# Kernel optimization log

Hardware: AMD Instinct MI355X
Metric: run time of the kernel (lower is better)

## Reference

```python
import jax, jax.numpy as jnp
import numpy as np

TAU = 2.0        # spikingjelly LIFNode default tau
ALPHA = 4.0      # sigmoid surrogate alpha (spikingjelly default)
NUM_HEADS = 8
CHUNK = 2

@jax.custom_vjp
def heaviside(x):
    return (x >= 0).astype(x.dtype)

def _h_fwd(x):
    return heaviside(x), x

def _h_bwd(x, g):
    s = jax.nn.sigmoid(ALPHA * x)
    return (g * ALPHA * s * (1.0 - s),)

heaviside.defvjp(_h_fwd, _h_bwd)

def lif(x, v_th):
    # multi-step LIF: v <- v + (x - v)/tau ; spike = H(v - v_th) ; hard reset to 0
    def step(v, xt):
        v = v + (xt - v) / TAU
        s = heaviside(v - v_th)
        return v * (1.0 - s), s
    _, spikes = jax.lax.scan(step, jnp.zeros_like(x[0]), x)
    return spikes

def bn(x, p, eps=1e-5):
    # eval-mode BatchNorm1d over channel dim C of [T,B,C,V]; p = [gamma,beta,mean,var] each [C]
    g, b, m, v = p[0], p[1], p[2], p[3]
    scale = g * jax.lax.rsqrt(v + eps)
    return (x - m[:, None]) * scale[:, None] + b[:, None]

def setup_inputs() -> dict:
    key = jax.random.key(0)
    T, B, C, V = 8, 16, 256, 1024
    ks = jax.random.split(key, 10)
    def mk_bn(k):
        k1, k2, k3, k4 = jax.random.split(k, 4)
        return jnp.stack([
            jax.random.uniform(k1, (C,)) + 0.5,          # gamma
            0.1 * jax.random.normal(k2, (C,)),           # beta
            0.1 * jax.random.normal(k3, (C,)),           # running mean
            jax.random.uniform(k4, (C,)) * 0.5 + 0.5,    # running var (>0)
        ])
    w_scale = C ** -0.5
    return {
        "x": jax.random.normal(ks[0], (T, B, C, V), jnp.float32),
        "q_w": w_scale * jax.random.normal(ks[1], (C, C), jnp.float32),
        "k_w": w_scale * jax.random.normal(ks[2], (C, C), jnp.float32),
        "v_w": w_scale * jax.random.normal(ks[3], (C, C), jnp.float32),
        "proj_w": w_scale * jax.random.normal(ks[4], (C, C), jnp.float32),
        "proj_b": 0.01 * jax.random.normal(ks[5], (C,), jnp.float32),
        "bn_q": mk_bn(ks[6]),
        "bn_k": mk_bn(ks[7]),
        "bn_v": mk_bn(ks[8]),
        "bn_proj": mk_bn(ks[9]),
    }

def reference(x, q_w, k_w, v_w, proj_w, proj_b, bn_q, bn_k, bn_v, bn_proj):
    T, B, C, V = x.shape
    H = NUM_HEADS
    D = C // H
    N = V
    NC = T // CHUNK
    identity = x

    xs = lif(x, 1.0)  # shortcut_lif

    def branch(w, bnp):
        y = jnp.einsum('oc,tbcv->tbov', w, xs)   # 1x1 conv
        y = lif(bn(y, bnp), 1.0)
        # [T,B,C,V] -> [T,B,H,N,D]
        return y.transpose(0, 1, 3, 2).reshape(T, B, N, H, D).transpose(0, 1, 3, 2, 4)

    q = branch(q_w, bn_q)
    k = branch(k_w, bn_k)
    v = branch(v_w, bn_v)

    def chunk(t):
        # [T,B,H,N,D] -> [NC,B,H,CHUNK*N,D]
        return (t.reshape(NC, CHUNK, B, H, N, D)
                 .transpose(0, 2, 3, 1, 4, 5)
                 .reshape(NC, B, H, CHUNK * N, D))

    qc, kc, vc = chunk(q), chunk(k), chunk(v)
    attn = jnp.einsum('nbhld,nbhle->nbhde', kc, vc) * (1.0 / N)  # [NC,B,H,D,D]
    out = jnp.einsum('nbhld,nbhde->nbhle', qc, attn)             # [NC,B,H,CHUNK*N,D]
    out = (out.reshape(NC, B, H, CHUNK, N, D)
              .transpose(0, 3, 1, 2, 4, 5)
              .reshape(T, B, H, N, D))

    y = out.transpose(0, 1, 2, 4, 3).reshape(T, B, C, N)  # [T,B,H,D,N] -> [T,B,C,N]
    y = lif(y, 0.5)  # attn_lif
    y = jnp.einsum('oc,tbcv->tbov', proj_w, y) + proj_b[None, None, :, None]
    y = bn(y, bn_proj)
    return y + identity, v
```

## Files before the change

kernel.cpp:

```cpp
#include <hip/hip_runtime.h>
#include <hip/hip_bf16.h>
#include <math.h>

typedef __bf16 bf16_t;
typedef __bf16 bf16x8 __attribute__((ext_vector_type(8)));
typedef __bf16 bf16x4 __attribute__((ext_vector_type(4)));
typedef float  f32x4  __attribute__((ext_vector_type(4)));

#define T_ 8
#define B_ 16
#define C_ 256
#define V_ 1024
#define H_ 8
#define D_ 32

#define MFMA __builtin_amdgcn_mfma_f32_16x16x32_bf16

__global__ __launch_bounds__(256) void k0_split4(const float* __restrict__ W0,
                                                 const float* __restrict__ W1,
                                                 const float* __restrict__ W2,
                                                 const float* __restrict__ W3,
                                                 bf16_t* __restrict__ S)
{
    const int mat = blockIdx.x >> 6;
    const float* W = (mat == 0) ? W0 : (mat == 1) ? W1 : (mat == 2) ? W2 : W3;
    bf16_t* S0 = S + (size_t)mat * 3 * 65536;
    bf16_t* S1 = S0 + 65536;
    bf16_t* S2 = S0 + 131072;
    int i = ((blockIdx.x & 63) * 256 + threadIdx.x) * 4;
    float4 w = *(const float4*)(W + i);
    float wv[4] = {w.x, w.y, w.z, w.w};
    bf16x4 s0, s1, s2;
#pragma unroll
    for (int j = 0; j < 4; j++) {
        bf16_t a = (bf16_t)wv[j];
        float r1 = wv[j] - (float)a;
        bf16_t b = (bf16_t)r1;
        float r2 = r1 - (float)b;
        bf16_t c = (bf16_t)r2;
        s0[j] = a; s1[j] = b; s2[j] = c;
    }
    *(bf16x4*)(S0 + i) = s0;
    *(bf16x4*)(S1 + i) = s1;
    *(bf16x4*)(S2 + i) = s2;
}

__global__ __launch_bounds__(256) void k1_lif_tr(const float* __restrict__ x,
                                                 bf16_t* __restrict__ xsT)
{
    __shared__ bf16_t tile[64 * 72];
    const int v0 = blockIdx.x * 64, c0 = blockIdx.y * 64, b = blockIdx.z;
    const int tid = threadIdx.x;
    const int cc = tid >> 2, v16 = (tid & 3) * 16;
    const int vr = tid >> 2, c16 = (tid & 3) * 16;
    float mem[16];
#pragma unroll
    for (int j = 0; j < 16; j++) mem[j] = 0.0f;

    for (int t = 0; t < T_; t++) {
        const float* xp = x + (((size_t)(t * B_ + b) * C_ + (c0 + cc)) * V_ + v0 + v16);
        float xv[16];
#pragma unroll
        for (int q = 0; q < 4; q++) {
            float4 f = *(const float4*)(xp + q * 4);
            xv[q * 4 + 0] = f.x; xv[q * 4 + 1] = f.y;
            xv[q * 4 + 2] = f.z; xv[q * 4 + 3] = f.w;
        }
#pragma unroll
        for (int j = 0; j < 16; j++) {
            float m = mem[j];
            float d = xv[j] - m;
            m = m + d * 0.5f;
            float s = (m >= 1.0f) ? 1.0f : 0.0f;
            tile[(v16 + j) * 72 + cc] = (bf16_t)s;
            mem[j] = (s != 0.0f) ? 0.0f : m;
        }
        __syncthreads();
        bf16_t* op = xsT + (((size_t)(t * B_ + b) * V_ + (v0 + vr)) * C_ + c0 + c16);
        *(bf16x8*)op       = *(const bf16x8*)&tile[vr * 72 + c16];
        *(bf16x8*)(op + 8) = *(const bf16x8*)&tile[vr * 72 + c16 + 8];
        __syncthreads();
    }
}

template <int ORIENT>
__global__ __launch_bounds__(256, 2) void k_branch(const bf16_t* __restrict__ Wsp,
                                                   const float* __restrict__ bnp,
                                                   const bf16_t* __restrict__ xsT,
                                                   bf16_t* __restrict__ outp, float vth)
{
    __shared__ bf16_t Wl[3][64 * 40];
    __shared__ bf16_t Xl[8][64 * 40];
    __shared__ float bsc[64], bmn[64], bbt[64];
    const int v0 = blockIdx.x * 64, o0 = blockIdx.y * 64, b = blockIdx.z;
    const int tid = threadIdx.x;
    const int w = tid >> 6, l = tid & 63, lq = l >> 4, lr = l & 15;
    const int msub = (w >> 1) * 32, nsub = (w & 1) * 32;

    if (tid < 64) {
        int o = o0 + tid;
        float g = bnp[o], be = bnp[C_ + o];
        float mn = bnp[2 * C_ + o], vr2 = bnp[3 * C_ + o];
        bsc[tid] = g * (1.0f / sqrtf(vr2 + 1e-5f));
        bmn[tid] = mn; bbt[tid] = be;
    }

    f32x4 acc[8][4];
#pragma unroll
    for (int t = 0; t < 8; t++)
#pragma unroll
        for (int i = 0; i < 4; i++) acc[t][i] = (f32x4){0.f, 0.f, 0.f, 0.f};

    for (int kq = 0; kq < 8; kq++) {
        __syncthreads();
#pragma unroll
        for (int i = 0; i < 3; i++) {
            int ch = tid + i * 256;
            int lvl = ch >> 8, rem = ch & 255;
            int row = rem >> 2, col8 = (rem & 3) * 8;
            *(bf16x8*)&Wl[lvl][row * 40 + col8] =
                *(const bf16x8*)&Wsp[lvl * 65536 + (o0 + row) * 256 + kq * 32 + col8];
        }
#pragma unroll
        for (int i = 0; i < 8; i++) {
            int ch = tid + i * 256;
            int tt = ch >> 8, rem = ch & 255;
            int row = rem >> 2, col8 = (rem & 3) * 8;
            *(bf16x8*)&Xl[tt][row * 40 + col8] =
                *(const bf16x8*)&xsT[((size_t)(tt * B_ + b) * V_ + v0 + row) * C_ + kq * 32 + col8];
        }
        __syncthreads();

        bf16x8 aw0[3], aw1[3];
#pragma unroll
        for (int lvl = 0; lvl < 3; lvl++) {
            aw0[lvl] = *(const bf16x8*)&Wl[lvl][(msub + lr) * 40 + lq * 8];
            aw1[lvl] = *(const bf16x8*)&Wl[lvl][(msub + 16 + lr) * 40 + lq * 8];
        }
#pragma unroll
        for (int t = 0; t < 8; t++) {
            bf16x8 b0 = *(const bf16x8*)&Xl[t][(nsub + lr) * 40 + lq * 8];
            bf16x8 b1 = *(const bf16x8*)&Xl[t][(nsub + 16 + lr) * 40 + lq * 8];
#pragma unroll
            for (int lvl = 0; lvl < 3; lvl++) {
                if (ORIENT == 0) {
                    acc[t][0] = MFMA(aw0[lvl], b0, acc[t][0], 0, 0, 0);
                    acc[t][1] = MFMA(aw0[lvl], b1, acc[t][1], 0, 0, 0);
                    acc[t][2] = MFMA(aw1[lvl], b0, acc[t][2], 0, 0, 0);
                    acc[t][3] = MFMA(aw1[lvl], b1, acc[t][3], 0, 0, 0);
                } else {
                    acc[t][0] = MFMA(b0, aw0[lvl], acc[t][0], 0, 0, 0);
                    acc[t][1] = MFMA(b1, aw0[lvl], acc[t][1], 0, 0, 0);
                    acc[t][2] = MFMA(b0, aw1[lvl], acc[t][2], 0, 0, 0);
                    acc[t][3] = MFMA(b1, aw1[lvl], acc[t][3], 0, 0, 0);
                }
            }
        }
    }

    __syncthreads();
    bf16_t* tl = (bf16_t*)Xl;
    const int orow = tid >> 2, ocol = (tid & 3) * 16;
    float mem[4][4];
#pragma unroll
    for (int st = 0; st < 4; st++)
#pragma unroll
        for (int r = 0; r < 4; r++) mem[st][r] = 0.0f;
#pragma unroll
    for (int t = 0; t < 8; t++) {
#pragma unroll
        for (int st = 0; st < 4; st++) {
            int mi = st >> 1, ni = st & 1;
#pragma unroll
            for (int r = 0; r < 4; r++) {
                int m, n;
                if (ORIENT == 0) {
                    m = msub + mi * 16 + lq * 4 + r;
                    n = nsub + ni * 16 + lr;
                } else {
                    m = msub + mi * 16 + lr;
                    n = nsub + ni * 16 + lq * 4 + r;
                }
                float y = (acc[t][st][r] - bmn[m]) * bsc[m] + bbt[m];
                float mm = mem[st][r];
                mm = mm + (y - mm) * 0.5f;
                float s = (mm >= vth) ? 1.0f : 0.0f;
                mem[st][r] = (s != 0.0f) ? 0.0f : mm;
                if (ORIENT == 0) tl[m * 72 + n] = (bf16_t)s;
                else             tl[n * 72 + m] = (bf16_t)s;
            }
        }
        __syncthreads();
        size_t rowbase;
        if (ORIENT == 0)
            rowbase = ((size_t)(t * B_ + b) * C_ + (o0 + orow)) * V_ + v0 + ocol;
        else
            rowbase = ((size_t)(t * B_ + b) * V_ + (v0 + orow)) * C_ + o0 + ocol;
        *(bf16x8*)&outp[rowbase]     = *(const bf16x8*)&tl[orow * 72 + ocol];
        *(bf16x8*)&outp[rowbase + 8] = *(const bf16x8*)&tl[orow * 72 + ocol + 8];
        __syncthreads();
    }
}

__global__ __launch_bounds__(256) void k_attn(const bf16_t* __restrict__ vc,
                                              const bf16_t* __restrict__ kc,
                                              bf16_t* __restrict__ ahi,
                                              bf16_t* __restrict__ alo)
{
    __shared__ float red[3][64][20];
    const int fid = blockIdx.x;
    const int h = fid & 7, b = (fid >> 3) & 15, nc = fid >> 7;
    const int tid = threadIdx.x, w = tid >> 6, l = tid & 63, lq = l >> 4, lr = l & 15;
    f32x4 acc[4];
#pragma unroll
    for (int i = 0; i < 4; i++) acc[i] = (f32x4){0.f, 0.f, 0.f, 0.f};
    for (int ss = 0; ss < 16; ss++) {
        int s = w * 16 + ss;
        int t = nc * 2 + (s >> 5);
        int n0 = (s & 31) * 32;
        size_t rb = ((size_t)(t * B_ + b) * C_ + h * D_ + lr) * V_ + n0 + lq * 8;
        bf16x8 a0 = *(const bf16x8*)&vc[rb];
        bf16x8 a1 = *(const bf16x8*)&vc[rb + (size_t)16 * V_];
        bf16x8 b0 = *(const bf16x8*)&kc[rb];
        bf16x8 b1 = *(const bf16x8*)&kc[rb + (size_t)16 * V_];
        acc[0] = MFMA(a0, b0, acc[0], 0, 0, 0);
        acc[1] = MFMA(a0, b1, acc[1], 0, 0, 0);
        acc[2] = MFMA(a1, b0, acc[2], 0, 0, 0);
        acc[3] = MFMA(a1, b1, acc[3], 0, 0, 0);
    }
    if (w) {
#pragma unroll
        for (int st = 0; st < 4; st++)
            *(f32x4*)&red[w - 1][l][st * 4] = acc[st];
    }
    __syncthreads();
    if (w == 0) {
#pragma unroll
        for (int st = 0; st < 4; st++)
#pragma unroll
            for (int i = 0; i < 3; i++)
                acc[st] += *(const f32x4*)&red[i][l][st * 4];

        size_t ob = (size_t)fid * 1024;
#pragma unroll
        for (int st = 0; st < 4; st++) {
            int ei = st >> 1, di = st & 1;
#pragma unroll
            for (int r = 0; r < 4; r++) {
                int e = ei * 16 + lq * 4 + r;
                int d = di * 16 + lr;
                float val = acc[st][r] * (1.0f / 1024.0f);
                bf16_t hi = (bf16_t)val;
                float lo = val - (float)hi;
                ahi[ob + e * 32 + d] = hi;
                alo[ob + e * 32 + d] = (bf16_t)lo;
            }
        }
    }
}

__global__ __launch_bounds__(256) void k_attn_out(const bf16_t* __restrict__ qT,
                                                  const bf16_t* __restrict__ ahi,
                                                  const bf16_t* __restrict__ alo,
                                                  bf16_t* __restrict__ y3T)
{
    const int tid = threadIdx.x, w = tid >> 6, l = tid & 63, lq = l >> 4, lr = l & 15;
    const int n0 = blockIdx.x * 64 + (w >> 1) * 32;
    const int h = blockIdx.y * 2 + (w & 1);
    const int b = blockIdx.z;
    float mem[4][4];
#pragma unroll
    for (int st = 0; st < 4; st++)
#pragma unroll
        for (int r = 0; r < 4; r++) mem[st][r] = 0.0f;

    for (int t = 0; t < T_; t++) {
        int nc = t >> 1;
        const bf16_t* qp = qT + ((size_t)(t * B_ + b) * V_ + n0 + lr) * C_ + h * D_ + lq * 8;
        bf16x8 a0 = *(const bf16x8*)qp;
        bf16x8 a1 = *(const bf16x8*)(qp + 16 * C_);
        size_t ab = ((size_t)(nc * B_ + b) * H_ + h) * 1024;
        bf16x8 bh0 = *(const bf16x8*)&ahi[ab + lr * 32 + lq * 8];
        bf16x8 bh1 = *(const bf16x8*)&ahi[ab + (16 + lr) * 32 + lq * 8];
        bf16x8 bl0 = *(const bf16x8*)&alo[ab + lr * 32 + lq * 8];
        bf16x8 bl1 = *(const bf16x8*)&alo[ab + (16 + lr) * 32 + lq * 8];
#pragma unroll
        for (int st = 0; st < 4; st++) {
            int mi = st >> 1, ni = st & 1;
            f32x4 z = (f32x4){0.f, 0.f, 0.f, 0.f};
            z = MFMA(mi ? a1 : a0, ni ? bh1 : bh0, z, 0, 0, 0);
            z = MFMA(mi ? a1 : a0, ni ? bl1 : bl0, z, 0, 0, 0);
#pragma unroll
            for (int r = 0; r < 4; r++) {
                int n = n0 + mi * 16 + lq * 4 + r;
                int e = ni * 16 + lr;
                float mm = mem[st][r];
                mm = mm + (z[r] - mm) * 0.5f;
                float s = (mm >= 0.5f) ? 1.0f : 0.0f;
                y3T[((size_t)(t * B_ + b) * V_ + n) * C_ + h * D_ + e] = (bf16_t)s;
                mem[st][r] = (s != 0.0f) ? 0.0f : mm;
            }
        }
    }
}

__global__ __launch_bounds__(256, 2) void k_proj(const bf16_t* __restrict__ Wsp,
                                                 const float* __restrict__ pb,
                                                 const float* __restrict__ bnp,
                                                 const bf16_t* __restrict__ y3T,
                                                 const float* __restrict__ x,
                                                 float* __restrict__ out0)
{
    __shared__ bf16_t Wl[3][64 * 40];
    __shared__ bf16_t Xl[8][64 * 40];
    __shared__ float bsc[64], bmn[64], bbt[64], bbi[64];
    const int v0 = blockIdx.x * 64, o0 = blockIdx.y * 64, b = blockIdx.z;
    const int tid = threadIdx.x;
    const int w = tid >> 6, l = tid & 63, lq = l >> 4, lr = l & 15;
    const int msub = (w >> 1) * 32, nsub = (w & 1) * 32;

    if (tid < 64) {
        int o = o0 + tid;
        float g = bnp[o], be = bnp[C_ + o];
        float mn = bnp[2 * C_ + o], vr2 = bnp[3 * C_ + o];
        bsc[tid] = g * (1.0f / sqrtf(vr2 + 1e-5f));
        bmn[tid] = mn; bbt[tid] = be; bbi[tid] = pb[o];
    }

    f32x4 acc[8][4];
#pragma unroll
    for (int t = 0; t < 8; t++)
#pragma unroll
        for (int i = 0; i < 4; i++) acc[t][i] = (f32x4){0.f, 0.f, 0.f, 0.f};

    for (int kq = 0; kq < 8; kq++) {
        __syncthreads();
#pragma unroll
        for (int i = 0; i < 3; i++) {
            int ch = tid + i * 256;
            int lvl = ch >> 8, rem = ch & 255;
            int row = rem >> 2, col8 = (rem & 3) * 8;
            *(bf16x8*)&Wl[lvl][row * 40 + col8] =
                *(const bf16x8*)&Wsp[lvl * 65536 + (o0 + row) * 256 + kq * 32 + col8];
        }
#pragma unroll
        for (int i = 0; i < 8; i++) {
            int ch = tid + i * 256;
            int tt = ch >> 8, rem = ch & 255;
            int row = rem >> 2, col8 = (rem & 3) * 8;
            *(bf16x8*)&Xl[tt][row * 40 + col8] =
                *(const bf16x8*)&y3T[((size_t)(tt * B_ + b) * V_ + v0 + row) * C_ + kq * 32 + col8];
        }
        __syncthreads();

        bf16x8 aw0[3], aw1[3];
#pragma unroll
        for (int lvl = 0; lvl < 3; lvl++) {
            aw0[lvl] = *(const bf16x8*)&Wl[lvl][(msub + lr) * 40 + lq * 8];
            aw1[lvl] = *(const bf16x8*)&Wl[lvl][(msub + 16 + lr) * 40 + lq * 8];
        }
#pragma unroll
        for (int t = 0; t < 8; t++) {
            bf16x8 b0 = *(const bf16x8*)&Xl[t][(nsub + lr) * 40 + lq * 8];
            bf16x8 b1 = *(const bf16x8*)&Xl[t][(nsub + 16 + lr) * 40 + lq * 8];
#pragma unroll
            for (int lvl = 0; lvl < 3; lvl++) {
                acc[t][0] = MFMA(aw0[lvl], b0, acc[t][0], 0, 0, 0);
                acc[t][1] = MFMA(aw0[lvl], b1, acc[t][1], 0, 0, 0);
                acc[t][2] = MFMA(aw1[lvl], b0, acc[t][2], 0, 0, 0);
                acc[t][3] = MFMA(aw1[lvl], b1, acc[t][3], 0, 0, 0);
            }
        }
    }

    __syncthreads();
    float* tf = (float*)Xl;
    const int orow = tid >> 2, ocol = (tid & 3) * 16;
#pragma unroll
    for (int t = 0; t < 8; t++) {
#pragma unroll
        for (int st = 0; st < 4; st++) {
            int mi = st >> 1, ni = st & 1;
#pragma unroll
            for (int r = 0; r < 4; r++) {
                int m = msub + mi * 16 + lq * 4 + r;
                int n = nsub + ni * 16 + lr;
                float y = acc[t][st][r] + bbi[m];
                y = (y - bmn[m]) * bsc[m] + bbt[m];
                tf[m * 68 + n] = y;
            }
        }
        __syncthreads();
        size_t rowbase = ((size_t)(t * B_ + b) * C_ + (o0 + orow)) * V_ + v0 + ocol;
#pragma unroll
        for (int q = 0; q < 4; q++) {
            float4 xv = *(const float4*)&x[rowbase + q * 4];
            float4 yv = *(const float4*)&tf[orow * 68 + ocol + q * 4];
            yv.x += xv.x; yv.y += xv.y; yv.z += xv.z; yv.w += xv.w;
            *(float4*)&out0[rowbase + q * 4] = yv;
        }
        __syncthreads();
    }
}

__global__ __launch_bounds__(256) void k_vout(const bf16_t* __restrict__ vc,
                                              float* __restrict__ out1)
{
    __shared__ bf16_t tl[32 * 136];
    const int n0 = blockIdx.x * 128;
    const int f = blockIdx.y;
    const int tb = f >> 3, h = f & 7;
    const int tid = threadIdx.x;
    {
        int d = tid >> 3, nn = (tid & 7) * 16;
        const bf16_t* vp = vc + ((size_t)tb * C_ + h * D_ + d) * V_ + n0 + nn;
        *(bf16x8*)&tl[d * 136 + nn]     = *(const bf16x8*)vp;
        *(bf16x8*)&tl[d * 136 + nn + 8] = *(const bf16x8*)(vp + 8);
    }
    __syncthreads();
    {
        int n = tid >> 1, d16 = (tid & 1) * 16;
        float* op = out1 + (size_t)f * (V_ * D_) + (size_t)(n0 + n) * D_ + d16;
#pragma unroll
        for (int q = 0; q < 4; q++) {
            float4 o;
            o.x = (float)tl[(d16 + q * 4 + 0) * 136 + n];
            o.y = (float)tl[(d16 + q * 4 + 1) * 136 + n];
            o.z = (float)tl[(d16 + q * 4 + 2) * 136 + n];
            o.w = (float)tl[(d16 + q * 4 + 3) * 136 + n];
            *(float4*)(op + q * 4) = o;
        }
    }
}

extern "C" void kernel_launch(void* const* d_in, const int* in_sizes, int n_in,
                              void* d_out, int out_size, void* d_ws, size_t ws_size,
                              hipStream_t stream)
{
    const float* x    = (const float*)d_in[0];
    const float* q_w  = (const float*)d_in[1];
    const float* k_w  = (const float*)d_in[2];
    const float* v_w  = (const float*)d_in[3];
    const float* pw   = (const float*)d_in[4];
    const float* pb   = (const float*)d_in[5];
    const float* bn_q = (const float*)d_in[6];
    const float* bn_k = (const float*)d_in[7];
    const float* bn_v = (const float*)d_in[8];
    const float* bn_p = (const float*)d_in[9];

    char* ws = (char*)d_ws;
    bf16_t* xsT  = (bf16_t*)(ws);
    bf16_t* vc   = (bf16_t*)(ws + ((size_t)64 << 20));
    bf16_t* ahi  = (bf16_t*)(ws + ((size_t)128 << 20));
    bf16_t* alo  = (bf16_t*)(ws + ((size_t)129 << 20));
    bf16_t* wspq = (bf16_t*)(ws + ((size_t)130 << 20));
    bf16_t* wspk = wspq + 3 * 65536;
    bf16_t* wspv = wspk + 3 * 65536;
    bf16_t* wspp = wspv + 3 * 65536;
    bf16_t* y3T  = xsT;

    float* outf = (float*)d_out;
    bf16_t* qT = (bf16_t*)d_out;
    bf16_t* kc = (bf16_t*)((char*)d_out + ((size_t)64 << 20));

    k0_split4  <<<dim3(256),        256, 0, stream>>>(q_w, k_w, v_w, pw, wspq);
    k1_lif_tr  <<<dim3(16, 4, 16),  256, 0, stream>>>(x, xsT);
    k_branch<1><<<dim3(16, 4, 16),  256, 0, stream>>>(wspq, bn_q, xsT, qT, 1.0f);
    k_branch<0><<<dim3(16, 4, 16),  256, 0, stream>>>(wspk, bn_k, xsT, kc, 1.0f);
    k_branch<0><<<dim3(16, 4, 16),  256, 0, stream>>>(wspv, bn_v, xsT, vc, 1.0f);
    k_attn     <<<dim3(512),        256, 0, stream>>>(vc, kc, ahi, alo);
    k_attn_out <<<dim3(16, 4, 16),  256, 0, stream>>>(qT, ahi, alo, y3T);
    k_proj     <<<dim3(16, 4, 16),  256, 0, stream>>>(wspp, pb, bn_p, y3T, x, outf);
    k_vout     <<<dim3(8, 1024),    256, 0, stream>>>(vc, outf + (size_t)33554432);
}
```

Baseline: 696.5 us.

## Load MFMA operands directly from global memory instead of LDS staging

In the branch and projection GEMM kernels, the shared-memory staging of weight and spike tiles is removed. Each wave now loads its MFMA A/B fragments straight from global memory (bf16x8 per lane), and the two barriers per K-step are dropped. Shared memory shrinks to just the epilogue transpose tile, which could allow more blocks per CU. In exchange, each operand is fetched redundantly by several waves, and the loads are strided 16-byte row accesses that rely on L1/L2 hits rather than coalesced LDS fills.

After: 893.3 us. 28.2% more time.

```diff
diff --git a/kernel.cpp b/kernel.cpp
--- a/kernel.cpp
+++ b/kernel.cpp
@@ -89,8 +89,7 @@
                                                    const bf16_t* __restrict__ xsT,
                                                    bf16_t* __restrict__ outp, float vth)
 {
-    __shared__ bf16_t Wl[3][64 * 40];
-    __shared__ bf16_t Xl[8][64 * 40];
+    __shared__ bf16_t tl[64 * 72];
     __shared__ float bsc[64], bmn[64], bbt[64];
     const int v0 = blockIdx.x * 64, o0 = blockIdx.y * 64, b = blockIdx.z;
     const int tid = threadIdx.x;
@@ -111,36 +110,24 @@
 #pragma unroll
         for (int i = 0; i < 4; i++) acc[t][i] = (f32x4){0.f, 0.f, 0.f, 0.f};
 
+    const bf16_t* wr0 = Wsp + (o0 + msub + lr) * 256;
+    const bf16_t* wr1 = Wsp + (o0 + msub + 16 + lr) * 256;
+    const size_t xrow0 = ((size_t)v0 + nsub + lr) * C_;
+    const size_t xrow1 = ((size_t)v0 + nsub + 16 + lr) * C_;
+
     for (int kq = 0; kq < 8; kq++) {
-        __syncthreads();
-#pragma unroll
-        for (int i = 0; i < 3; i++) {
-            int ch = tid + i * 256;
-            int lvl = ch >> 8, rem = ch & 255;
-            int row = rem >> 2, col8 = (rem & 3) * 8;
-            *(bf16x8*)&Wl[lvl][row * 40 + col8] =
-                *(const bf16x8*)&Wsp[lvl * 65536 + (o0 + row) * 256 + kq * 32 + col8];
-        }
-#pragma unroll
-        for (int i = 0; i < 8; i++) {
-            int ch = tid + i * 256;
-            int tt = ch >> 8, rem = ch & 255;
-            int row = rem >> 2, col8 = (rem & 3) * 8;
-            *(bf16x8*)&Xl[tt][row * 40 + col8] =
-                *(const bf16x8*)&xsT[((size_t)(tt * B_ + b) * V_ + v0 + row) * C_ + kq * 32 + col8];
-        }
-        __syncthreads();
-
+        const int kc8 = kq * 32 + lq * 8;
         bf16x8 aw0[3], aw1[3];
 #pragma unroll
         for (int lvl = 0; lvl < 3; lvl++) {
-            aw0[lvl] = *(const bf16x8*)&Wl[lvl][(msub + lr) * 40 + lq * 8];
-            aw1[lvl] = *(const bf16x8*)&Wl[lvl][(msub + 16 + lr) * 40 + lq * 8];
+            aw0[lvl] = *(const bf16x8*)&wr0[lvl * 65536 + kc8];
+            aw1[lvl] = *(const bf16x8*)&wr1[lvl * 65536 + kc8];
         }
 #pragma unroll
         for (int t = 0; t < 8; t++) {
-            bf16x8 b0 = *(const bf16x8*)&Xl[t][(nsub + lr) * 40 + lq * 8];
-            bf16x8 b1 = *(const bf16x8*)&Xl[t][(nsub + 16 + lr) * 40 + lq * 8];
+            const bf16_t* xb = xsT + (size_t)(t * B_ + b) * (V_ * C_) + kc8;
+            bf16x8 b0 = *(const bf16x8*)&xb[xrow0];
+            bf16x8 b1 = *(const bf16x8*)&xb[xrow1];
 #pragma unroll
             for (int lvl = 0; lvl < 3; lvl++) {
                 if (ORIENT == 0) {
@@ -158,8 +145,6 @@
         }
     }
 
-    __syncthreads();
-    bf16_t* tl = (bf16_t*)Xl;
     const int orow = tid >> 2, ocol = (tid & 3) * 16;
     float mem[4][4];
 #pragma unroll
@@ -311,8 +296,7 @@
                                                  const float* __restrict__ x,
                                                  float* __restrict__ out0)
 {
-    __shared__ bf16_t Wl[3][64 * 40];
-    __shared__ bf16_t Xl[8][64 * 40];
+    __shared__ float tf[64 * 68];
     __shared__ float bsc[64], bmn[64], bbt[64], bbi[64];
     const int v0 = blockIdx.x * 64, o0 = blockIdx.y * 64, b = blockIdx.z;
     const int tid = threadIdx.x;
@@ -333,36 +317,24 @@
 #pragma unroll
         for (int i = 0; i < 4; i++) acc[t][i] = (f32x4){0.f, 0.f, 0.f, 0.f};
 
+    const bf16_t* wr0 = Wsp + (o0 + msub + lr) * 256;
+    const bf16_t* wr1 = Wsp + (o0 + msub + 16 + lr) * 256;
+    const size_t xrow0 = ((size_t)v0 + nsub + lr) * C_;
+    const size_t xrow1 = ((size_t)v0 + nsub + 16 + lr) * C_;
+
     for (int kq = 0; kq < 8; kq++) {
-        __syncthreads();
-#pragma unroll
-        for (int i = 0; i < 3; i++) {
-            int ch = tid + i * 256;
-            int lvl = ch >> 8, rem = ch & 255;
-            int row = rem >> 2, col8 = (rem & 3) * 8;
-            *(bf16x8*)&Wl[lvl][row * 40 + col8] =
-                *(const bf16x8*)&Wsp[lvl * 65536 + (o0 + row) * 256 + kq * 32 + col8];
-        }
-#pragma unroll
-        for (int i = 0; i < 8; i++) {
-            int ch = tid + i * 256;
-            int tt = ch >> 8, rem = ch & 255;
-            int row = rem >> 2, col8 = (rem & 3) * 8;
-            *(bf16x8*)&Xl[tt][row * 40 + col8] =
-                *(const bf16x8*)&y3T[((size_t)(tt * B_ + b) * V_ + v0 + row) * C_ + kq * 32 + col8];
-        }
-        __syncthreads();
-
+        const int kc8 = kq * 32 + lq * 8;
         bf16x8 aw0[3], aw1[3];
 #pragma unroll
         for (int lvl = 0; lvl < 3; lvl++) {
-            aw0[lvl] = *(const bf16x8*)&Wl[lvl][(msub + lr) * 40 + lq * 8];
-            aw1[lvl] = *(const bf16x8*)&Wl[lvl][(msub + 16 + lr) * 40 + lq * 8];
+            aw0[lvl] = *(const bf16x8*)&wr0[lvl * 65536 + kc8];
+            aw1[lvl] = *(const bf16x8*)&wr1[lvl * 65536 + kc8];
         }
 #pragma unroll
         for (int t = 0; t < 8; t++) {
-            bf16x8 b0 = *(const bf16x8*)&Xl[t][(nsub + lr) * 40 + lq * 8];
-            bf16x8 b1 = *(const bf16x8*)&Xl[t][(nsub + 16 + lr) * 40 + lq * 8];
+            const bf16_t* xb = y3T + (size_t)(t * B_ + b) * (V_ * C_) + kc8;
+            bf16x8 b0 = *(const bf16x8*)&xb[xrow0];
+            bf16x8 b1 = *(const bf16x8*)&xb[xrow1];
 #pragma unroll
             for (int lvl = 0; lvl < 3; lvl++) {
                 acc[t][0] = MFMA(aw0[lvl], b0, acc[t][0], 0, 0, 0);
@@ -373,8 +345,6 @@
         }
     }
 
-    __syncthreads();
-    float* tf = (float*)Xl;
     const int orow = tid >> 2, ocol = (tid & 3) * 16;
 #pragma unroll
     for (int t = 0; t < 8; t++) {
```
